# Kernel tuning notes

Measured on AMD Instinct MI355X. Metric: run time of the kernel, lower is better.

## Reference

```python
import jax, jax.numpy as jnp
import numpy as np

B, R, L, K, E, H, V, QV = 256, 6, 10, 49, 300, 512, 2001, 10000


def _lstm_dir(x, Wih, Whh, bih, bhh):
    # x: [N, L, E]; returns final hidden state [N, H] (PyTorch gate order i,f,g,o)
    N = x.shape[0]
    Hd = Whh.shape[1]
    b = bih + bhh

    def step(carry, xt):
        h, c = carry
        gates = xt @ Wih.T + h @ Whh.T + b
        i, f, g, o = jnp.split(gates, 4, axis=-1)
        c = jax.nn.sigmoid(f) * c + jax.nn.sigmoid(i) * jnp.tanh(g)
        h = jax.nn.sigmoid(o) * jnp.tanh(c)
        return (h, c), None

    init = (jnp.zeros((N, Hd), x.dtype), jnp.zeros((N, Hd), x.dtype))
    (h, _), _ = jax.lax.scan(step, init, jnp.swapaxes(x, 0, 1))
    return h


def setup_inputs() -> dict:
    key = jax.random.key(0)
    ks = jax.random.split(key, 40)
    s = 0.02
    d = {}
    d['img'] = jax.random.normal(ks[0], (B * R, K, H), jnp.float32)
    d['role_qs'] = jax.random.randint(ks[1], (B, R, L), 0, QV, jnp.int64)
    d['qword_emb'] = jax.random.normal(ks[2], (QV, E), jnp.float32) * s
    d['lstm_Wih_f'] = jax.random.normal(ks[3], (4 * H, E), jnp.float32) * s
    d['lstm_Whh_f'] = jax.random.normal(ks[4], (4 * H, H), jnp.float32) * s
    d['lstm_bih_f'] = jnp.zeros((4 * H,), jnp.float32)
    d['lstm_bhh_f'] = jnp.zeros((4 * H,), jnp.float32)
    d['lstm_Wih_b'] = jax.random.normal(ks[5], (4 * H, E), jnp.float32) * s
    d['lstm_Whh_b'] = jax.random.normal(ks[6], (4 * H, H), jnp.float32) * s
    d['lstm_bih_b'] = jnp.zeros((4 * H,), jnp.float32)
    d['lstm_bhh_b'] = jnp.zeros((4 * H,), jnp.float32)
    d['proj_W'] = jax.random.normal(ks[7], (H, 2 * H), jnp.float32) * s
    d['proj_b'] = jnp.zeros((H,), jnp.float32)
    d['vatt_vW'] = jax.random.normal(ks[8], (H, H), jnp.float32) * s
    d['vatt_vb'] = jnp.zeros((H,), jnp.float32)
    d['vatt_qW'] = jax.random.normal(ks[9], (H, H), jnp.float32) * s
    d['vatt_qb'] = jnp.zeros((H,), jnp.float32)
    d['vatt_oW'] = jax.random.normal(ks[10], (1, H), jnp.float32) * s
    d['vatt_ob'] = jnp.zeros((1,), jnp.float32)
    d['qnet_W'] = jax.random.normal(ks[11], (H, H), jnp.float32) * s
    d['qnet_b'] = jnp.zeros((H,), jnp.float32)
    d['vnet_W'] = jax.random.normal(ks[12], (H, H), jnp.float32) * s
    d['vnet_b'] = jnp.zeros((H,), jnp.float32)
    d['cls_W1'] = jax.random.normal(ks[13], (2 * H, H), jnp.float32) * s
    d['cls_b1'] = jnp.zeros((2 * H,), jnp.float32)
    d['cls_W2'] = jax.random.normal(ks[14], (V, 2 * H), jnp.float32) * s
    d['cls_b2'] = jnp.zeros((V,), jnp.float32)
    d['g0_W'] = jax.random.normal(ks[15], (H, 2 * H), jnp.float32) * s
    d['g0_b'] = jnp.zeros((H,), jnp.float32)
    d['g1_W'] = jax.random.normal(ks[16], (H, H), jnp.float32) * s
    d['g1_b'] = jnp.zeros((H,), jnp.float32)
    d['g2_W'] = jax.random.normal(ks[17], (H, H), jnp.float32) * s
    d['g2_b'] = jnp.zeros((H,), jnp.float32)
    d['g3_W'] = jax.random.normal(ks[18], (H, H), jnp.float32) * s
    d['g3_b'] = jnp.zeros((H,), jnp.float32)
    d['f0_W'] = jax.random.normal(ks[19], (H, H), jnp.float32) * s
    d['f0_b'] = jnp.zeros((H,), jnp.float32)
    d['f1_W'] = jax.random.normal(ks[20], (H, H), jnp.float32) * s
    d['f1_b'] = jnp.zeros((H,), jnp.float32)
    return d


def _forward(img, qword_emb,
             lstm_Wih_f, lstm_Whh_f, lstm_bih_f, lstm_bhh_f,
             lstm_Wih_b, lstm_Whh_b, lstm_bih_b, lstm_bhh_b,
             proj_W, proj_b, vatt_vW, vatt_vb, vatt_qW, vatt_qb, vatt_oW, vatt_ob,
             qnet_W, qnet_b, vnet_W, vnet_b, cls_W1, cls_b1, cls_W2, cls_b2,
             g0_W, g0_b, g1_W, g1_b, g2_W, g2_b, g3_W, g3_b,
             f0_W, f0_b, f1_W, f1_b, role_qs):
    relu = jax.nn.relu
    bsz, roles = role_qs.shape[0], role_qs.shape[1]
    toks = role_qs.reshape(-1, role_qs.shape[-1])          # [B*R, L]
    w_emb = qword_emb[toks]                                 # [B*R, L, E]
    # bidirectional LSTM final hidden states
    h_f = _lstm_dir(w_emb, lstm_Wih_f, lstm_Whh_f, lstm_bih_f, lstm_bhh_f)
    h_b = _lstm_dir(w_emb[:, ::-1, :], lstm_Wih_b, lstm_Whh_b, lstm_bih_b, lstm_bhh_b)
    q_emb = jnp.concatenate([h_f, h_b], axis=-1) @ proj_W.T + proj_b   # [B*R, H]
    # top-down attention over image regions
    v_proj = relu(img @ vatt_vW.T + vatt_vb)                # [B*R, K, H]
    q_proj = relu(q_emb @ vatt_qW.T + vatt_qb)              # [B*R, H]
    att_logits = (v_proj * q_proj[:, None, :]) @ vatt_oW.T + vatt_ob  # [B*R, K, 1]
    att = jax.nn.softmax(att_logits, axis=1)
    v_emb = jnp.sum(att * img, axis=1)                      # [B*R, H]
    # joint representation + answer classifier
    q_repr = relu(q_emb @ qnet_W.T + qnet_b)
    v_repr = relu(v_emb @ vnet_W.T + vnet_b)
    joint_repr = q_repr * v_repr                            # [B*R, H]
    logits = relu(joint_repr @ cls_W1.T + cls_b1) @ cls_W2.T + cls_b2  # [B*R, V]
    # relation network over pairwise role representations
    jr = joint_repr.reshape(bsz, roles, -1)                 # [B, R, H]
    r1 = jnp.broadcast_to(jr[:, None, :, :], (bsz, roles, roles, jr.shape[-1]))
    r2 = jnp.broadcast_to(jr[:, :, None, :], (bsz, roles, roles, jr.shape[-1]))
    cat = jnp.concatenate([r1, r2], axis=-1).reshape(-1, 2 * jr.shape[-1])  # [B*R*R, 2H]
    g = relu(cat @ g0_W.T + g0_b)
    g = relu(g @ g1_W.T + g1_b)
    g = relu(g @ g2_W.T + g2_b)
    g = relu(g @ g3_W.T + g3_b)
    g = g.reshape(bsz, roles * roles, -1).sum(axis=1)       # [B, H]
    rec = relu(g @ f0_W.T + f0_b) @ f1_W.T + f1_b           # [B, H]
    rec = rec / jnp.sqrt(jnp.sum(rec * rec, axis=1, keepdims=True))  # l2norm
    return logits, rec


def reference(img, role_qs, qword_emb,
              lstm_Wih_f, lstm_Whh_f, lstm_bih_f, lstm_bhh_f,
              lstm_Wih_b, lstm_Whh_b, lstm_bih_b, lstm_bhh_b,
              proj_W, proj_b, vatt_vW, vatt_vb, vatt_qW, vatt_qb, vatt_oW, vatt_ob,
              qnet_W, qnet_b, vnet_W, vnet_b, cls_W1, cls_b1, cls_W2, cls_b2,
              g0_W, g0_b, g1_W, g1_b, g2_W, g2_b, g3_W, g3_b,
              f0_W, f0_b, f1_W, f1_b):
    return _forward(img, qword_emb,
                    lstm_Wih_f, lstm_Whh_f, lstm_bih_f, lstm_bhh_f,
                    lstm_Wih_b, lstm_Whh_b, lstm_bih_b, lstm_bhh_b,
                    proj_W, proj_b, vatt_vW, vatt_vb, vatt_qW, vatt_qb, vatt_oW, vatt_ob,
                    qnet_W, qnet_b, vnet_W, vnet_b, cls_W1, cls_b1, cls_W2, cls_b2,
                    g0_W, g0_b, g1_W, g1_b, g2_W, g2_b, g3_W, g3_b,
                    f0_W, f0_b, f1_W, f1_b, role_qs)
```

## Files before the change

kernel.cpp:

```cpp
#include <hip/hip_runtime.h>
#include <hip/hip_bf16.h>
#include <math.h>

typedef __attribute__((ext_vector_type(8))) short short8;
typedef __attribute__((ext_vector_type(4))) float f32x4;

#define KTILE 32
#define LSTR 40
#define LSTR64 72

__device__ __forceinline__ short8 cvt8(const float* x) {
    short8 r;
#pragma unroll
    for (int i = 0; i < 8; ++i) {
        __hip_bfloat16 b = __float2bfloat16(x[i]);
        r[i] = *reinterpret_cast<const short*>(&b);
    }
    return r;
}
__device__ __forceinline__ float bf2f(short s) {
    unsigned int u = ((unsigned int)(unsigned short)s) << 16;
    return __uint_as_float(u);
}
__device__ __forceinline__ void gload16(const void* g, void* l) {
// ... 50 lines not shown
#pragma unroll
        for (int n = 0; n < 2; ++n) acc[m][n] = (f32x4){0.f, 0.f, 0.f, 0.f};

    short8 aS0, aS1, wS;
    auto loadA = [&](int t) {
        constexpr int AE = (BM == 128) ? 16 : 8;
        const int k0 = t * KTILE + kA;
        if (k0 + AE <= k1) {
            if (abits & 1) {
                const short* p = A1b + (size_t)rgA * lda1 + k0;
                aS0 = *(const short8*)p;
                if constexpr (BM == 128) aS1 = *(const short8*)(p + 8);
            } else {
                const float* p = A1f + (size_t)rgA * lda1 + k0;
                float4 v0 = *(const float4*)p, v1 = *(const float4*)(p + 4);
                float t0[8] = {v0.x, v0.y, v0.z, v0.w, v1.x, v1.y, v1.z, v1.w};
                aS0 = cvt8(t0);
                if constexpr (BM == 128) {
                    float4 v2 = *(const float4*)(p + 8), v3 = *(const float4*)(p + 12);
                    float t1[8] = {v2.x, v2.y, v2.z, v2.w, v3.x, v3.y, v3.z, v3.w};
                    aS1 = cvt8(t1);
                }
            }
        } else if (k0 >= k1 && k0 + AE <= Ktot) {
            const int kk = k0 - k1;
            if (abits & 2) {
                const short* p = A2b + (size_t)rgA * lda2 + kk;
                aS0 = *(const short8*)p;
                if constexpr (BM == 128) aS1 = *(const short8*)(p + 8);
            } else {
                const float* p = A2f + (size_t)rgA * lda2 + kk;
                float4 v0 = *(const float4*)p, v1 = *(const float4*)(p + 4);
                float t0[8] = {v0.x, v0.y, v0.z, v0.w, v1.x, v1.y, v1.z, v1.w};
                aS0 = cvt8(t0);
                if constexpr (BM == 128) {
                    float4 v2 = *(const float4*)(p + 8), v3 = *(const float4*)(p + 12);
                    float t1[8] = {v2.x, v2.y, v2.z, v2.w, v3.x, v3.y, v3.z, v3.w};
                    aS1 = cvt8(t1);
                }
            }
        } else {
            float tmp[(BM == 128) ? 16 : 8];
#pragma unroll
            for (int e = 0; e < ((BM == 128) ? 16 : 8); ++e) {
                const int kg = k0 + e;
                float v = 0.f;
                if (kg < k1) v = (abits & 1) ? bf2f(A1b[(size_t)rgA * lda1 + kg]) : A1f[(size_t)rgA * lda1 + kg];
                else if (kg < Ktot) v = (abits & 2) ? bf2f(A2b[(size_t)rgA * lda2 + (kg - k1)]) : A2f[(size_t)rgA * lda2 + (kg - k1)];
                tmp[e] = v;
            }
            aS0 = cvt8(tmp);
            if constexpr (BM == 128) aS1 = cvt8(tmp + 8);
        }
    };
    auto loadW = [&](int t) {
        const int k0 = t * KTILE + kW;
        if (k0 + 8 <= k1) {
            wS = *(const short8*)&W1[(size_t)ngW * ldw1 + k0];
        } else if (k0 >= k1 && k0 + 8 <= Ktot) {
            wS = *(const short8*)&W2[(size_t)ngW * ldw2 + (k0 - k1)];
        } else {
            short8 w;
#pragma unroll
            for (int e = 0; e < 8; ++e) {
                const int kg = k0 + e;
                w[e] = (kg < k1) ? W1[(size_t)ngW * ldw1 + kg]
                                 : ((kg < Ktot) ? W2[(size_t)ngW * ldw2 + (kg - k1)] : (short)0);
            }
            wS = w;
        }
    };
    auto writeS = [&](int buf) {
        *(short8*)&sA[buf][rowA][kA] = aS0;
        if constexpr (BM == 128) *(short8*)&sA[buf][rowA][kA + 8] = aS1;
        *(short8*)&sB[buf][rowW][kW] = wS;
    };

    loadA(0); loadW(0); writeS(0);
    __syncthreads();
    for (int t = 0; t < nt; ++t) {
        const int cur = t & 1;
        if (t + 1 < nt) { loadA(t + 1); loadW(t + 1); }
        short8 af[MF], bfv[2];
#pragma unroll
        for (int m = 0; m < MF; ++m)
            af[m] = *(const short8*)&sA[cur][wr + (m << 4) + l15][lh << 3];
#pragma unroll
        for (int n = 0; n < 2; ++n)
            bfv[n] = *(const short8*)&sB[cur][wc + (n << 4) + l15][lh << 3];
#pragma unroll
        for (int m = 0; m < MF; ++m)
#pragma unroll
            for (int n = 0; n < 2; ++n)
                acc[m][n] = __builtin_amdgcn_mfma_f32_16x16x32_bf16(af[m], bfv[n], acc[m][n], 0, 0, 0);
        if (t + 1 < nt) writeS(cur ^ 1);
        __syncthreads();
    }

    if (mode == 0) {
#pragma unroll
        for (int m = 0; m < MF; ++m) {
#pragma unroll
            for (int j = 0; j < 4; ++j) {
                const int r = m0 + wr + (m << 4) + (lh << 2) + j;
                if (r >= M) continue;
#pragma unroll
                for (int n = 0; n < 2; ++n) {
                    const int c = n0 + wc + (n << 4) + l15;
                    if (c >= N) continue;
                    float v = acc[m][n][j];
                    if (bias1) v += bias1[c];
                    if (do_relu) v = fmaxf(v, 0.f);
                    if (mulvec) v *= mulvec[c];
                    if (mul) v *= mul[(size_t)r * ldc + c];
                    if (c_bf16) {
                        __hip_bfloat16 b = __float2bfloat16(v);
                        ((short*)C)[(size_t)r * ldc + c] = *(short*)&b;
                    } else {
                        C[(size_t)r * ldc + c] = v;
                    }
                }
            }
        }
    } else {
#pragma unroll
        for (int m = 0; m < MF; ++m) {
#pragma unroll
            for (int j = 0; j < 4; ++j) {
                const int rloc = wr + (m << 4) + (lh << 2) + j;
                const int r = m0 + rloc;
                const size_t sqbase = (size_t)(r / 49) * ldc;
                float s = 0.f;
#pragma unroll
                for (int n = 0; n < 2; ++n) {
                    const int c = n0 + wc + (n << 4) + l15;
                    float v = acc[m][n][j] + bias1[c];
                    v = fmaxf(v, 0.f);
                    s += v * mul[sqbase + c];
                }
                s += __shfl_xor(s, 1, 64);
                s += __shfl_xor(s, 2, 64);
                s += __shfl_xor(s, 4, 64);
                s += __shfl_xor(s, 8, 64);
                if (l15 == 0) sred[rloc][wc >> 5] = s;
            }
        }
        __syncthreads();
        if (tid < BM)
            C[(size_t)(m0 + tid) * 8 + ch8] = sred[tid][0] + sred[tid][1];
    }
}

__global__ __launch_bounds__(256)
void attn_logits3_kernel(const short* __restrict__ imgb, const short* __restrict__ vW,
                         const float* __restrict__ vb, const float* __restrict__ swq,
                         float* __restrict__ partial)
{
    __shared__ short sA[2][128][64];
    __shared__ short sB[2][64][64];
    __shared__ float sred[128][2];
    const int tid = threadIdx.x;
    const int lane = tid & 63, wave = tid >> 6;
    const int xcd = blockIdx.x & 7;
    const int gi = xcd * 588 + (blockIdx.x >> 3);
    const int m0 = (gi >> 3) << 7;
    const int ch8 = gi & 7;
    const int n0 = ch8 << 6;
    const int wr = (wave >> 1) << 6;
    const int wc = (wave & 1) << 5;
    const int l15 = lane & 15, lh = lane >> 4;
    const int lr = lane >> 3;
    const int sc = (lane & 7) ^ lr;

    f32x4 acc[4][2];
#pragma unroll
    for (int m = 0; m < 4; ++m)
#pragma unroll
        for (int n = 0; n < 2; ++n) acc[m][n] = (f32x4){0.f, 0.f, 0.f, 0.f};

    auto stage = [&](int t, int buf) {
        const int kb = t << 6;
#pragma unroll
        for (int j = 0; j < 4; ++j) {
            const int r0 = (wave << 5) + (j << 3);
            const int grow = m0 + r0 + lr;
            gload16(imgb + (size_t)grow * 512 + kb + (sc << 3), &sA[buf][r0][0]);
        }
#pragma unroll
        for (int j = 0; j < 2; ++j) {
            const int r0 = (wave << 4) + (j << 3);
            const int grow = n0 + r0 + lr;
            gload16(vW + (size_t)grow * 512 + kb + (sc << 3), &sB[buf][r0][0]);
        }
    };

    stage(0, 0);
    __syncthreads();
    for (int t = 0; t < 8; ++t) {
        const int cur = t & 1;
        if (t + 1 < 8) stage(t + 1, cur ^ 1);
#pragma unroll
        for (int kk = 0; kk < 2; ++kk) {
            const int rd = (((kk << 2) + lh) ^ (l15 & 7)) << 3;
            short8 af[4], bfv[2];
#pragma unroll
            for (int m = 0; m < 4; ++m)
                af[m] = *(const short8*)&sA[cur][wr + (m << 4) + l15][rd];
#pragma unroll
            for (int n = 0; n < 2; ++n)
                bfv[n] = *(const short8*)&sB[cur][wc + (n << 4) + l15][rd];
#pragma unroll
            for (int m = 0; m < 4; ++m)
#pragma unroll
                for (int n = 0; n < 2; ++n)
                    acc[m][n] = __builtin_amdgcn_mfma_f32_16x16x32_bf16(af[m], bfv[n], acc[m][n], 0, 0, 0);
        }
        __syncthreads();
    }

#pragma unroll
    for (int m = 0; m < 4; ++m) {
#pragma unroll
        for (int j = 0; j < 4; ++j) {
            const int rloc = wr + (m << 4) + (lh << 2) + j;
            const int r = m0 + rloc;
            const size_t sqbase = (size_t)(r / 49) * 512;
            float s = 0.f;
#pragma unroll
            for (int n = 0; n < 2; ++n) {
                const int c = n0 + wc + (n << 4) + l15;
                float v = acc[m][n][j] + vb[c];
                v = fmaxf(v, 0.f);
                s += v * swq[sqbase + c];
            }
            s += __shfl_xor(s, 1, 64);
            s += __shfl_xor(s, 2, 64);
            s += __shfl_xor(s, 4, 64);
            s += __shfl_xor(s, 8, 64);
            if (l15 == 0) sred[rloc][wc >> 5] = s;
        }
    }
    __syncthreads();
    if (tid < 128)
        partial[(size_t)(m0 + tid) * 8 + ch8] = sred[tid][0] + sred[tid][1];
}

__global__ __launch_bounds__(256)
void mfma_gemm64_kernel(const float* __restrict__ A1f, int lda1, int k1,
                        const short* __restrict__ W1, int ldw1,
                        const float* __restrict__ A2f, int lda2, int k2,
                        const short* __restrict__ W2, int ldw2,
                        const float* __restrict__ bias1,
                        const float* __restrict__ mulvec, const float* __restrict__ mul,
                        float* __restrict__ C, int ldc, int M, int N,
                        int do_relu, int abits, int c_bf16)
{
    __shared__ short sA[2][64][LSTR64];
    __shared__ short sB[2][64][LSTR64];
    const int tid = threadIdx.x;
    const int m0 = blockIdx.y << 6, n0 = blockIdx.x << 6;
    const short* A1b = (const short*)A1f;
    const short* A2b = (const short*)A2f;
    const int Ktot = k1 + k2;
    const int nt = (Ktot + 63) >> 6;
    const int lane = tid & 63, wave = tid >> 6;
    const int wr = (wave >> 1) << 5, wc = (wave & 1) << 5;
    const int l15 = lane & 15, lh = lane >> 4;
    const int srow = tid >> 2, skq = (tid & 3) << 4;
    const int rgA = min(m0 + srow, M - 1);
    const int ngW = min(n0 + srow, N - 1);

    f32x4 acc[2][2];
#pragma unroll
    for (int m = 0; m < 2; ++m)
#pragma unroll
        for (int n = 0; n < 2; ++n) acc[m][n] = (f32x4){0.f, 0.f, 0.f, 0.f};

    short8 aS0, aS1, wS0, wS1;
    auto loadA = [&](int t) {
        const int k0 = (t << 6) + skq;
        if (k0 + 16 <= k1) {
            if (abits & 1) {
                const short* p = A1b + (size_t)rgA * lda1 + k0;
                aS0 = *(const short8*)p; aS1 = *(const short8*)(p + 8);
            } else {
                const float* p = A1f + (size_t)rgA * lda1 + k0;
                float4 v0 = *(const float4*)p, v1 = *(const float4*)(p + 4);
                float4 v2 = *(const float4*)(p + 8), v3 = *(const float4*)(p + 12);
                float t0[8] = {v0.x, v0.y, v0.z, v0.w, v1.x, v1.y, v1.z, v1.w};
                float t1[8] = {v2.x, v2.y, v2.z, v2.w, v3.x, v3.y, v3.z, v3.w};
                aS0 = cvt8(t0); aS1 = cvt8(t1);
            }
        } else if (k0 >= k1 && k0 + 16 <= Ktot) {
            const int kk = k0 - k1;
            if (abits & 2) {
                const short* p = A2b + (size_t)rgA * lda2 + kk;
                aS0 = *(const short8*)p; aS1 = *(const short8*)(p + 8);
            } else {
                const float* p = A2f + (size_t)rgA * lda2 + kk;
                float4 v0 = *(const float4*)p, v1 = *(const float4*)(p + 4);
                float4 v2 = *(const float4*)(p + 8), v3 = *(const float4*)(p + 12);
                float t0[8] = {v0.x, v0.y, v0.z, v0.w, v1.x, v1.y, v1.z, v1.w};
                float t1[8] = {v2.x, v2.y, v2.z, v2.w, v3.x, v3.y, v3.z, v3.w};
                aS0 = cvt8(t0); aS1 = cvt8(t1);
            }
        } else {
            float tmp[16];
#pragma unroll
            for (int e = 0; e < 16; ++e) {
                const int kg = k0 + e;
                float v = 0.f;
                if (kg < k1) v = (abits & 1) ? bf2f(A1b[(size_t)rgA * lda1 + kg]) : A1f[(size_t)rgA * lda1 + kg];
                else if (kg < Ktot) v = (abits & 2) ? bf2f(A2b[(size_t)rgA * lda2 + (kg - k1)]) : A2f[(size_t)rgA * lda2 + (kg - k1)];
                tmp[e] = v;
            }
            aS0 = cvt8(tmp); aS1 = cvt8(tmp + 8);
        }
    };
    auto loadW = [&](int t) {
        const int k0 = (t << 6) + skq;
        if (k0 + 16 <= k1) {
            const short* p = W1 + (size_t)ngW * ldw1 + k0;
            wS0 = *(const short8*)p; wS1 = *(const short8*)(p + 8);
        } else if (k0 >= k1 && k0 + 16 <= Ktot) {
            const short* p = W2 + (size_t)ngW * ldw2 + (k0 - k1);
            wS0 = *(const short8*)p; wS1 = *(const short8*)(p + 8);
        } else {
            short8 w0, w1;
#pragma unroll
            for (int e = 0; e < 16; ++e) {
                const int kg = k0 + e;
                short v = (kg < k1) ? W1[(size_t)ngW * ldw1 + kg]
                                    : ((kg < Ktot) ? W2[(size_t)ngW * ldw2 + (kg - k1)] : (short)0);
                if (e < 8) w0[e] = v; else w1[e - 8] = v;
            }
            wS0 = w0; wS1 = w1;
        }
    };
    auto writeS = [&](int buf) {
        *(short8*)&sA[buf][srow][skq] = aS0;
        *(short8*)&sA[buf][srow][skq + 8] = aS1;
        *(short8*)&sB[buf][srow][skq] = wS0;
        *(short8*)&sB[buf][srow][skq + 8] = wS1;
    };

    loadA(0); loadW(0); writeS(0);
    __syncthreads();
    for (int t = 0; t < nt; ++t) {
        const int cur = t & 1;
        if (t + 1 < nt) { loadA(t + 1); loadW(t + 1); }
#pragma unroll
        for (int kk = 0; kk < 2; ++kk) {
            short8 af[2], bfv[2];
#pragma unroll
            for (int m = 0; m < 2; ++m)
                af[m] = *(const short8*)&sA[cur][wr + (m << 4) + l15][(kk << 5) + (lh << 3)];
#pragma unroll
            for (int n = 0; n < 2; ++n)
                bfv[n] = *(const short8*)&sB[cur][wc + (n << 4) + l15][(kk << 5) + (lh << 3)];
#pragma unroll
            for (int m = 0; m < 2; ++m)
#pragma unroll
                for (int n = 0; n < 2; ++n)
                    acc[m][n] = __builtin_amdgcn_mfma_f32_16x16x32_bf16(af[m], bfv[n], acc[m][n], 0, 0, 0);
        }
        if (t + 1 < nt) writeS(cur ^ 1);
        __syncthreads();
    }

#pragma unroll
    for (int m = 0; m < 2; ++m) {
#pragma unroll
        for (int j = 0; j < 4; ++j) {
            const int r = m0 + wr + (m << 4) + (lh << 2) + j;
            if (r >= M) continue;
#pragma unroll
            for (int n = 0; n < 2; ++n) {
                const int c = n0 + wc + (n << 4) + l15;
                if (c >= N) continue;
                float v = acc[m][n][j];
                if (bias1) v += bias1[c];
                if (do_relu) v = fmaxf(v, 0.f);
                if (mulvec) v *= mulvec[c];
                if (mul) v *= mul[(size_t)r * ldc + c];
                if (c_bf16) {
                    __hip_bfloat16 b = __float2bfloat16(v);
                    ((short*)C)[(size_t)r * ldc + c] = *(short*)&b;
                } else {
                    C[(size_t)r * ldc + c] = v;
                }
            }
        }
    }
}

__global__ __launch_bounds__(256)
void wcvt_kernel(const float* __restrict__ proj, const float* __restrict__ qW,
                 const float* __restrict__ vW, const float* __restrict__ qnet,
                 const float* __restrict__ vnet, const float* __restrict__ cls1,
                 const float* __restrict__ cls2, const float* __restrict__ g0,
                 const float* __restrict__ g1, const float* __restrict__ g2,
                 const float* __restrict__ g3, const float* __restrict__ f0,
                 const float* __restrict__ f1, short* __restrict__ dst)
{
    size_t idx = ((size_t)blockIdx.x * 256 + threadIdx.x) * 8;
    if (idx >= 5981184) return;
    const float* s;
    if (idx < 524288) s = proj + idx;
    else if (idx < 786432) s = qW + (idx - 524288);
    else if (idx < 1048576) s = vW + (idx - 786432);
    else if (idx < 1310720) s = qnet + (idx - 1048576);
    else if (idx < 1572864) s = vnet + (idx - 1310720);
    else if (idx < 2097152) s = cls1 + (idx - 1572864);
    else if (idx < 4146176) s = cls2 + (idx - 2097152);
    else if (idx < 4670464) {
        size_t li = idx - 4146176;
        int c = (int)(li >> 9), k = (int)(li & 511);
        s = (c < 512) ? g0 + (size_t)c * 1024 + k
                      : g0 + (size_t)(c - 512) * 1024 + 512 + k;
    }
    else if (idx < 4932608) s = g1 + (idx - 4670464);
    else if (idx < 5194752) s = g2 + (idx - 4932608);
    else if (idx < 5456896) s = g3 + (idx - 5194752);
    else if (idx < 5719040) s = f0 + (idx - 5456896);
    else s = f1 + (idx - 5719040);
    float4 a = *(const float4*)s, b = *(const float4*)(s + 4);
    float t[8] = {a.x, a.y, a.z, a.w, b.x, b.y, b.z, b.w};
    *(short8*)(dst + idx) = cvt8(t);
}

__global__ __launch_bounds__(256)
void lstm_reorder_kernel(const float* __restrict__ Wih, const float* __restrict__ Whh,
                         const float* __restrict__ bih, const float* __restrict__ bhh,
                         short* __restrict__ Wbf, float* __restrict__ bias_perm)
{
    int id = blockIdx.x * 256 + threadIdx.x;
    int c = id >> 9, k = id & 511;
    int src = (c & 3) * 512 + (c >> 2);
    {
        __hip_bfloat16 b = __float2bfloat16(Whh[(size_t)src * 512 + k]);
        Wbf[(size_t)c * 832 + k] = *(short*)&b;
    }
    if (k < 300) {
        __hip_bfloat16 b = __float2bfloat16(Wih[(size_t)src * 300 + k]);
        Wbf[(size_t)c * 832 + 512 + k] = *(short*)&b;
    } else if (k < 320) {
        Wbf[(size_t)c * 832 + 512 + k] = 0;
    }
    if (k == 0) bias_perm[c] = bih[src] + bhh[src];
}

__global__ __launch_bounds__(256)
void embcvt_kernel(const float* __restrict__ qword, short* __restrict__ embp)
{
    int id = blockIdx.x * 256 + threadIdx.x;
    if (id >= 3200000) return;
    int r = id / 320, c = id % 320;
    float v = (c < 300) ? qword[(size_t)r * 300 + c] : 0.f;
    __hip_bfloat16 b = __float2bfloat16(v);
    embp[id] = *(short*)&b;
}

__global__ __launch_bounds__(256)
void lstm_step6_kernel(const short* __restrict__ hF_in, const short* __restrict__ hB_in,
                       const short* __restrict__ WbfF, const short* __restrict__ WbfB,
                       const float* __restrict__ biasF, const float* __restrict__ biasB,
                       const short* __restrict__ embp, const int* __restrict__ toks,
                       int tF, int tB, int first,
                       short* __restrict__ hF_out, short* __restrict__ hB_out,
                       float* __restrict__ cF, float* __restrict__ cB)
{
    __shared__ short sA[2][64][64];
    __shared__ short sB[2][64][64];
    const int dir = blockIdx.z;
    const short* h_in = dir ? hB_in : hF_in;
    const short* Wbf  = dir ? WbfB : WbfF;
    const float* bias_perm = dir ? biasB : biasF;
    short* h_out  = dir ? hB_out : hF_out;
    float* cstate = dir ? cB : cF;
    const int tt = dir ? tB : tF;

    const int tid = threadIdx.x;
    const int m0 = blockIdx.y << 6;
    const int n0 = blockIdx.x << 6;
    const int lane = tid & 63, wave = tid >> 6;
    const int wr = (wave >> 1) << 5, wc = (wave & 1) << 5;
    const int l15 = lane & 15, lh = lane >> 4;
    const int lr = lane >> 3;
    const int sc = (lane & 7) ^ lr;

    f32x4 acc[2][2];
#pragma unroll
    for (int m = 0; m < 2; ++m)
#pragma unroll
        for (int n = 0; n < 2; ++n) acc[m][n] = (f32x4){0.f, 0.f, 0.f, 0.f};

    auto stage = [&](int t, int buf) {
#pragma unroll
        for (int j = 0; j < 2; ++j) {
            const int r0 = (wave << 4) + (j << 3);
            const int grow = m0 + r0 + lr;
            const short* g;
            if (t < 8) {
                g = h_in + (size_t)grow * 512 + (t << 6) + (sc << 3);
            } else {
                const int ar = toks[grow * 10 + tt];
                g = embp + (size_t)ar * 320 + ((t - 8) << 6) + (sc << 3);
            }
            gload16(g, &sA[buf][r0][0]);
        }
#pragma unroll
        for (int j = 0; j < 2; ++j) {
            const int r0 = (wave << 4) + (j << 3);
            const int grow = n0 + r0 + lr;
            gload16(Wbf + (size_t)grow * 832 + (t << 6) + (sc << 3), &sB[buf][r0][0]);
        }
    };

    stage(0, 0);
    __syncthreads();
    for (int t = 0; t < 13; ++t) {
        const int cur = t & 1;
        if (t + 1 < 13) stage(t + 1, cur ^ 1);
#pragma unroll
        for (int kk = 0; kk < 2; ++kk) {
            const int rd = (((kk << 2) + lh) ^ (l15 & 7)) << 3;
            short8 af[2], bfv[2];
#pragma unroll
            for (int m = 0; m < 2; ++m)
                af[m] = *(const short8*)&sA[cur][wr + (m << 4) + l15][rd];
#pragma unroll
            for (int n = 0; n < 2; ++n)
                bfv[n] = *(const short8*)&sB[cur][wc + (n << 4) + l15][rd];
#pragma unroll
            for (int m = 0; m < 2; ++m)
#pragma unroll
                for (int n = 0; n < 2; ++n)
                    acc[m][n] = __builtin_amdgcn_mfma_f32_16x16x32_bf16(af[m], bfv[n], acc[m][n], 0, 0, 0);
        }
        __syncthreads();
    }

#pragma unroll
    for (int n = 0; n < 2; ++n) {
        const int ccol = n0 + wc + (n << 4) + l15;
        const float bb = bias_perm[ccol];
        const int u = ccol >> 2;
#pragma unroll
        for (int m = 0; m < 2; ++m) {
#pragma unroll
            for (int j = 0; j < 4; ++j) {
                const int r = m0 + wr + (m << 4) + (lh << 2) + j;
                float v = acc[m][n][j] + bb;
                const int base = lane & ~3;
                float gi = __shfl(v, base, 64);
                float gf = __shfl(v, base | 1, 64);
                float gg = __shfl(v, base | 2, 64);
                float go = __shfl(v, base | 3, 64);
                if ((lane & 3) == 0) {
                    float si = 1.f / (1.f + expf(-gi));
                    float sf = 1.f / (1.f + expf(-gf));
                    float so = 1.f / (1.f + expf(-go));
                    size_t idx = ((size_t)r << 9) + u;
                    float cold = first ? 0.f : cstate[idx];
                    float cv = sf * cold + si * tanhf(gg);
                    cstate[idx] = cv;
                    float hv = so * tanhf(cv);
                    __hip_bfloat16 b = __float2bfloat16(hv);
                    h_out[idx] = *(short*)&b;
                }
            }
        }
    }
}

__global__ __launch_bounds__(256)
void lstm_step4_kernel(const short* __restrict__ hF_in, const short* __restrict__ hB_in,
                       const short* __restrict__ WbfF, const short* __restrict__ WbfB,
                       const float* __restrict__ biasF, const float* __restrict__ biasB,
                       const float* __restrict__ emb, const int* __restrict__ toks,
                       int tF, int tB, int first,
                       short* __restrict__ hF_out, short* __restrict__ hB_out,
                       float* __restrict__ cF, float* __restrict__ cB)
{
    __shared__ short sA[2][64][LSTR64];
    __shared__ short sB[2][64][LSTR64];
    const int dir = blockIdx.z;
    const short* h_in = dir ? hB_in : hF_in;
    const short* Wbf  = dir ? WbfB : WbfF;
    const float* bias_perm = dir ? biasB : biasF;
    short* h_out  = dir ? hB_out : hF_out;
    float* cstate = dir ? cB : cF;
    const int tt = dir ? tB : tF;

    const int tid = threadIdx.x;
    const int m0 = blockIdx.y << 6;
    const int n0 = blockIdx.x << 6;
    const int lane = tid & 63, wave = tid >> 6;
    const int wr = (wave >> 1) << 5, wc = (wave & 1) << 5;
    const int l15 = lane & 15, lh = lane >> 4;
    const int srow = tid >> 2, skq = (tid & 3) << 4;
    const int rgA = m0 + srow;
    const int ngW = n0 + srow;
    const int nt = 13;
    const int arow = toks[rgA * 10 + tt];

    f32x4 acc[2][2];
#pragma unroll
    for (int m = 0; m < 2; ++m)
#pragma unroll
        for (int n = 0; n < 2; ++n) acc[m][n] = (f32x4){0.f, 0.f, 0.f, 0.f};

    short8 aS0, aS1, wS0, wS1;
    auto loadA = [&](int t) {
        const int k0 = (t << 6) + skq;
        if (k0 + 16 <= 512) {
            if (first) { short8 z = {0,0,0,0,0,0,0,0}; aS0 = z; aS1 = z; }
            else {
                const short* p = h_in + (size_t)rgA * 512 + k0;
                aS0 = *(const short8*)p; aS1 = *(const short8*)(p + 8);
            }
        } else if (k0 >= 512 && k0 + 16 <= 812) {
            const float* p = emb + (size_t)arow * 300 + (k0 - 512);
            float4 v0 = *(const float4*)p, v1 = *(const float4*)(p + 4);
            float4 v2 = *(const float4*)(p + 8), v3 = *(const float4*)(p + 12);
            float t0[8] = {v0.x, v0.y, v0.z, v0.w, v1.x, v1.y, v1.z, v1.w};
            float t1[8] = {v2.x, v2.y, v2.z, v2.w, v3.x, v3.y, v3.z, v3.w};
            aS0 = cvt8(t0); aS1 = cvt8(t1);
        } else {
            float tmp[16];
#pragma unroll
            for (int e = 0; e < 16; ++e) {
                const int kg = k0 + e;
                float v = 0.f;
                if (kg < 512) v = first ? 0.f : bf2f(h_in[(size_t)rgA * 512 + kg]);
                else if (kg < 812) v = emb[(size_t)arow * 300 + (kg - 512)];
                tmp[e] = v;
            }
            aS0 = cvt8(tmp); aS1 = cvt8(tmp + 8);
        }
    };
    auto loadW = [&](int t) {
        const short* p = Wbf + (size_t)ngW * 832 + (t << 6) + skq;
        wS0 = *(const short8*)p; wS1 = *(const short8*)(p + 8);
    };
    auto writeS = [&](int buf) {
        *(short8*)&sA[buf][srow][skq] = aS0;
        *(short8*)&sA[buf][srow][skq + 8] = aS1;
        *(short8*)&sB[buf][srow][skq] = wS0;
        *(short8*)&sB[buf][srow][skq + 8] = wS1;
    };

    loadA(0); loadW(0); writeS(0);
    __syncthreads();
    for (int t = 0; t < nt; ++t) {
        const int cur = t & 1;
        if (t + 1 < nt) { loadA(t + 1); loadW(t + 1); }
#pragma unroll
        for (int kk = 0; kk < 2; ++kk) {
            short8 af[2], bfv[2];
#pragma unroll
            for (int m = 0; m < 2; ++m)
                af[m] = *(const short8*)&sA[cur][wr + (m << 4) + l15][(kk << 5) + (lh << 3)];
#pragma unroll
            for (int n = 0; n < 2; ++n)
                bfv[n] = *(const short8*)&sB[cur][wc + (n << 4) + l15][(kk << 5) + (lh << 3)];
#pragma unroll
            for (int m = 0; m < 2; ++m)
// ... 90 lines not shown
    }
    ((float2*)(v_emb + (size_t)n * 512))[tid] = s2;
}

__global__ __launch_bounds__(256)
void g0build_kernel(const float* __restrict__ PQ, const float* __restrict__ b0,
                    short* __restrict__ g0)
{
    int id = blockIdx.x * 256 + threadIdx.x;
    int cc = id & 511;
    int r = id >> 9;
    int j = r % 6;
    int t = r / 6;
    int i = t % 6;
    int b = t / 6;
    float v = PQ[(size_t)(b * 6 + j) * 1024 + cc] + PQ[(size_t)(b * 6 + i) * 1024 + 512 + cc] + b0[cc];
    v = fmaxf(v, 0.f);
    __hip_bfloat16 h = __float2bfloat16(v);
    g0[id] = *(short*)&h;
}

__global__ __launch_bounds__(256)
void gsum_kernel(const short* __restrict__ g, float* __restrict__ out)
{
    int id = blockIdx.x * 256 + threadIdx.x;
    int b = id >> 9, hh = id & 511;
    const short* p = g + (size_t)b * 36 * 512 + hh;
    float s = 0.f;
#pragma unroll
    for (int i = 0; i < 36; ++i) s += bf2f(p[i * 512]);
    out[id] = s;
}

__global__ __launch_bounds__(256)
void l2norm_kernel(const float* __restrict__ in, float* __restrict__ out)
{
    int b = blockIdx.x;
    int tid = threadIdx.x;
    float v0 = in[(size_t)b * 512 + tid];
    float v1 = in[(size_t)b * 512 + 256 + tid];
    float s = v0 * v0 + v1 * v1;
#pragma unroll
    for (int off = 32; off; off >>= 1) s += __shfl_down(s, off, 64);
    __shared__ float ps[4];
    if ((tid & 63) == 0) ps[tid >> 6] = s;
    __syncthreads();
    float tot = ps[0] + ps[1] + ps[2] + ps[3];
    float inv = 1.f / sqrtf(tot);
    out[(size_t)b * 512 + tid] = v0 * inv;
    out[(size_t)b * 512 + 256 + tid] = v1 * inv;
}

extern "C" void kernel_launch(void* const* d_in, const int* in_sizes, int n_in,
                              void* d_out, int out_size, void* d_ws, size_t ws_size,
                              hipStream_t stream)
{
    (void)in_sizes; (void)n_in; (void)out_size;
    const float* img    = (const float*)d_in[0];
    const int*   toks   = (const int*)d_in[1];
    const float* qword  = (const float*)d_in[2];
    const float* Wih_f  = (const float*)d_in[3];
    const float* Whh_f  = (const float*)d_in[4];
    const float* bih_f  = (const float*)d_in[5];
    const float* bhh_f  = (const float*)d_in[6];
    const float* Wih_b  = (const float*)d_in[7];
    const float* Whh_b  = (const float*)d_in[8];
    const float* bih_b  = (const float*)d_in[9];
    const float* bhh_b  = (const float*)d_in[10];
    const float* proj_W = (const float*)d_in[11];
    const float* proj_b = (const float*)d_in[12];
    const float* vatt_vW = (const float*)d_in[13];
    const float* vatt_vb = (const float*)d_in[14];
    const float* vatt_qW = (const float*)d_in[15];
    const float* vatt_qb = (const float*)d_in[16];
    const float* vatt_oW = (const float*)d_in[17];
    const float* qnet_W = (const float*)d_in[19];
    const float* qnet_b = (const float*)d_in[20];
    const float* vnet_W = (const float*)d_in[21];
    const float* vnet_b = (const float*)d_in[22];
    const float* cls_W1 = (const float*)d_in[23];
    const float* cls_b1 = (const float*)d_in[24];
    const float* cls_W2 = (const float*)d_in[25];
    const float* cls_b2 = (const float*)d_in[26];
    const float* g0_W   = (const float*)d_in[27];
    const float* g0_b   = (const float*)d_in[28];
    const float* g1_W   = (const float*)d_in[29];
    const float* g1_b   = (const float*)d_in[30];
    const float* g2_W   = (const float*)d_in[31];
    const float* g2_b   = (const float*)d_in[32];
    const float* g3_W   = (const float*)d_in[33];
    const float* g3_b   = (const float*)d_in[34];
    const float* f0_W   = (const float*)d_in[35];
    const float* f0_b   = (const float*)d_in[36];
    const float* f1_W   = (const float*)d_in[37];
    const float* f1_b   = (const float*)d_in[38];

    float* out_logits = (float*)d_out;
    float* out_rec    = (float*)d_out + 1536 * 2001;

    const size_t FB = 786432;
    float* zone = (float*)d_ws;
    float* gA    = zone;
    float* gB    = zone + 4718592;
    float* hid1  = zone + 9437184;
    float* PQb   = zone + 11010048;
    float* gsumb = zone + 12582912;
    float* f0o   = zone + 12713984;
    float* rectb = zone + 12845056;
    float* p = zone + 12976128;
    auto alloc = [&](size_t nf) { float* q = p; p += nf; return q; };
    float* hP0   = alloc(FB);
    float* hP2   = alloc(FB);
    float* joint = alloc(FB);
    float* partial = alloc(602112);
    short* WbfF  = (short*)alloc(851968);
    short* WbfB  = (short*)alloc(851968);
    float* biasF = alloc(2048);
    float* biasB = alloc(2048);
    const size_t TOPF = 17645568;
    short* wb = (short*)(zone + TOPF);
    short* projbf = wb;
    short* qWbf   = wb + 524288;
    short* vWbf   = wb + 786432;
    short* qnetbf = wb + 1048576;
    short* vnetbf = wb + 1310720;
    short* cls1bf = wb + 1572864;
    short* cls2bf = wb + 2097152;
    short* wpqbf  = wb + 4146176;
    short* g1bf   = wb + 4670464;
    short* g2bf   = wb + 4932608;
    short* g3bf   = wb + 5194752;
    short* f0bf   = wb + 5456896;
    short* f1bf   = wb + 5719040;
    const size_t WEND = TOPF + 2990592;
    const size_t IMGBF = 19267584;
    const size_t EMBPF = 1600000;
    const bool useimgbf = ws_size >= (WEND + IMGBF) * sizeof(float);
    const bool useglds  = ws_size >= (WEND + IMGBF + EMBPF) * sizeof(float);
    short* imgbf = (short*)(zone + WEND);
    short* embp  = (short*)(zone + WEND + IMGBF);
    short* hP1 = (short*)gA;
    short* hP3 = (short*)(gA + FB);
    float* cF  = gA + 2 * FB;
    float* cB  = gA + 3 * FB;
    float* q_emb  = PQb;
    float* swq    = hid1;
    float* q_repr = gA;
    float* v_emb  = gA + FB;

    auto gemm = [&](const float* A1, int lda1, int k1, const short* W1, int ldw1,
                    const float* A2, int lda2, int k2, const short* W2, int ldw2,
                    const float* b1, const float* mv, const float* mulp,
                    float* Cp, int ldc, int M, int N, int relu, int abits, int cbf) {
        if (M >= 4096) {
            dim3 g((N + 63) / 64, (M + 127) / 128);
            hipLaunchKernelGGL(HIP_KERNEL_NAME(mfma_gemm_t<128>), g, dim3(256), 0, stream,
                               A1, lda1, k1, W1, ldw1, A2, lda2, k2, W2, ldw2,
                               b1, mv, mulp, Cp, ldc, M, N, relu, 0, abits, cbf);
        } else {
            dim3 g((N + 63) / 64, (M + 63) / 64);
            hipLaunchKernelGGL(mfma_gemm64_kernel, g, dim3(256), 0, stream,
                               A1, lda1, k1, W1, ldw1, A2, lda2, k2, W2, ldw2,
                               b1, mv, mulp, Cp, ldc, M, N, relu, abits, cbf);
        }
    };

    const int NR = 1536;
    hipLaunchKernelGGL(lstm_reorder_kernel, dim3(4096), dim3(256), 0, stream,
                       Wih_f, Whh_f, bih_f, bhh_f, WbfF, biasF);
    hipLaunchKernelGGL(lstm_reorder_kernel, dim3(4096), dim3(256), 0, stream,
                       Wih_b, Whh_b, bih_b, bhh_b, WbfB, biasB);
    hipLaunchKernelGGL(wcvt_kernel, dim3(2921), dim3(256), 0, stream,
                       proj_W, vatt_qW, vatt_vW, qnet_W, vnet_W, cls_W1, cls_W2,
                       g0_W, g1_W, g2_W, g3_W, f0_W, f1_W, wb);
    if (useimgbf)
        hipLaunchKernelGGL(imgcvt_kernel, dim3(18816), dim3(256), 0, stream, img, imgbf);

    if (useglds) {
        hipLaunchKernelGGL(embcvt_kernel, dim3(12500), dim3(256), 0, stream, qword, embp);
        hipMemsetAsync(hP0, 0, FB * sizeof(short), stream);
        hipMemsetAsync(hP2, 0, FB * sizeof(short), stream);
        short *fi = (short*)hP0, *fo = hP1, *bi = (short*)hP2, *bo = hP3;
        for (int t = 0; t < 10; ++t) {
            hipLaunchKernelGGL(lstm_step6_kernel, dim3(32, 24, 2), dim3(256), 0, stream,
                               fi, bi, WbfF, WbfB, biasF, biasB, embp, toks, t, 9 - t,
                               (t == 0) ? 1 : 0, fo, bo, cF, cB);
            short* tmp = fi; fi = fo; fo = tmp;
            tmp = bi; bi = bo; bo = tmp;
        }
    } else {
        short *fi = (short*)hP0, *fo = hP1, *bi = (short*)hP2, *bo = hP3;
        for (int t = 0; t < 10; ++t) {
            hipLaunchKernelGGL(lstm_step4_kernel, dim3(32, 24, 2), dim3(256), 0, stream,
                               fi, bi, WbfF, WbfB, biasF, biasB, qword, toks, t, 9 - t,
                               (t == 0) ? 1 : 0, fo, bo, cF, cB);
            short* tmp = fi; fi = fo; fo = tmp;
            tmp = bi; bi = bo; bo = tmp;
        }
    }

    gemm(hP0, 512, 512, projbf, 1024, hP2, 512, 512, projbf + 512, 1024,
         proj_b, nullptr, nullptr, q_emb, 512, NR, 512, 0, 3, 1);
    gemm(q_emb, 512, 512, qWbf, 512, nullptr, 0, 0, nullptr, 0,
         vatt_qb, vatt_oW, nullptr, swq, 512, NR, 512, 1, 1, 0);
    if (useimgbf) {
        hipLaunchKernelGGL(attn_logits3_kernel, dim3(4704), dim3(256), 0, stream,
                           imgbf, vWbf, vatt_vb, swq, partial);
    } else {
        hipLaunchKernelGGL(HIP_KERNEL_NAME(mfma_gemm_t<128>), dim3(4704), dim3(256), 0, stream,
                           img, 512, 512, vWbf, 512,
                           (const float*)nullptr, 0, 0, (const short*)nullptr, 0,
                           vatt_vb, (const float*)nullptr, swq,
                           partial, 512, 75264, 512, 0, 1, 0, 0);
    }
    hipLaunchKernelGGL(attn_vemb_kernel, dim3(1536), dim3(256), 0, stream,
                       partial, img, useimgbf ? imgbf : (const short*)nullptr, v_emb);
    gemm(q_emb, 512, 512, qnetbf, 512, nullptr, 0, 0, nullptr, 0,
         qnet_b, nullptr, nullptr, q_repr, 512, NR, 512, 1, 1, 0);
    gemm(v_emb, 512, 512, vnetbf, 512, nullptr, 0, 0, nullptr, 0,
         vnet_b, nullptr, q_repr, joint, 512, NR, 512, 1, 0, 1);
    gemm(joint, 512, 512, cls1bf, 512, nullptr, 0, 0, nullptr, 0,
         cls_b1, nullptr, nullptr, hid1, 1024, NR, 1024, 1, 1, 1);
    gemm(hid1, 1024, 1024, cls2bf, 1024, nullptr, 0, 0, nullptr, 0,
         cls_b2, nullptr, nullptr, out_logits, 2001, NR, 2001, 0, 1, 0);
    gemm(joint, 512, 512, wpqbf, 512, nullptr, 0, 0, nullptr, 0,
         nullptr, nullptr, nullptr, PQb, 1024, NR, 1024, 0, 1, 0);
    hipLaunchKernelGGL(g0build_kernel, dim3(18432), dim3(256), 0, stream,
                       PQb, g0_b, (short*)gA);
    gemm(gA, 512, 512, g1bf, 512, nullptr, 0, 0, nullptr, 0,
         g1_b, nullptr, nullptr, gB, 512, 9216, 512, 1, 1, 1);
    gemm(gB, 512, 512, g2bf, 512, nullptr, 0, 0, nullptr, 0,
         g2_b, nullptr, nullptr, gA, 512, 9216, 512, 1, 1, 1);
    gemm(gA, 512, 512, g3bf, 512, nullptr, 0, 0, nullptr, 0,
         g3_b, nullptr, nullptr, gB, 512, 9216, 512, 1, 1, 1);
    hipLaunchKernelGGL(gsum_kernel, dim3(512), dim3(256), 0, stream, (const short*)gB, gsumb);
    gemm(gsumb, 512, 512, f0bf, 512, nullptr, 0, 0, nullptr, 0,
         f0_b, nullptr, nullptr, f0o, 512, 256, 512, 1, 0, 0);
    gemm(f0o, 512, 512, f1bf, 512, nullptr, 0, 0, nullptr, 0,
         f1_b, nullptr, nullptr, rectb, 512, 256, 512, 0, 0, 0);
    hipLaunchKernelGGL(l2norm_kernel, dim3(256), dim3(256), 0, stream, rectb, out_rec);
}
```

Before: 787.5 us.

## Route bf16-input GEMMs through direct global-to-LDS kernels and shrink attention tiles

Adds two GEMM kernels that take bf16 operands and stage tiles with direct global-to-LDS 16-byte loads and XOR swizzling, in 64x64 and 128x64 variants. Most mid-size linear layers (proj, qatt, qnet, cls1, PQ) and the three 9216-row relation MLP layers now use them instead of the generic float/bf16 GEMM path. The attention-logit kernel switches from 128-row to 64-row tiles, doubling the grid to improve occupancy and load balance. The generic gemm lambda now always uses the 64-tile kernel. This relies on the producers already writing bf16 and on M and N being multiples of the tile sizes.

```diff
diff --git a/kernel.cpp b/kernel.cpp
--- a/kernel.cpp
+++ b/kernel.cpp
@@ -226,45 +226,211 @@
 }
 
 __global__ __launch_bounds__(256)
-void attn_logits3_kernel(const short* __restrict__ imgb, const short* __restrict__ vW,
+void mfma_glds64_kernel(const short* __restrict__ A1, const short* __restrict__ A2,
+                        int lda, int k1, const short* __restrict__ W, int ldw,
+                        const float* __restrict__ bias, const float* __restrict__ mulvec,
+                        float* __restrict__ C, int ldc, int Ktot, int do_relu, int c_bf16)
+{
+    __shared__ short sA[2][64][64];
+    __shared__ short sB[2][64][64];
+    const int tid = threadIdx.x;
+    const int m0 = blockIdx.y << 6, n0 = blockIdx.x << 6;
+    const int lane = tid & 63, wave = tid >> 6;
+    const int wr = (wave >> 1) << 5, wc = (wave & 1) << 5;
+    const int l15 = lane & 15, lh = lane >> 4;
+    const int lr = lane >> 3;
+    const int sc = (lane & 7) ^ lr;
+    const int nt = Ktot >> 6;
+    const int t1 = k1 >> 6;
+
+    f32x4 acc[2][2];
+#pragma unroll
+    for (int m = 0; m < 2; ++m)
+#pragma unroll
+        for (int n = 0; n < 2; ++n) acc[m][n] = (f32x4){0.f, 0.f, 0.f, 0.f};
+
+    auto stage = [&](int t, int buf) {
+        const short* Ab = (t < t1) ? A1 : A2;
+        const int kb = ((t < t1) ? t : (t - t1)) << 6;
+#pragma unroll
+        for (int j = 0; j < 2; ++j) {
+            const int r0 = (wave << 4) + (j << 3);
+            gload16(Ab + (size_t)(m0 + r0 + lr) * lda + kb + (sc << 3), &sA[buf][r0][0]);
+        }
+#pragma unroll
+        for (int j = 0; j < 2; ++j) {
+            const int r0 = (wave << 4) + (j << 3);
+            gload16(W + (size_t)(n0 + r0 + lr) * ldw + (t << 6) + (sc << 3), &sB[buf][r0][0]);
+        }
+    };
+
+    stage(0, 0);
+    __syncthreads();
+    for (int t = 0; t < nt; ++t) {
+        const int cur = t & 1;
+        if (t + 1 < nt) stage(t + 1, cur ^ 1);
+#pragma unroll
+        for (int kk = 0; kk < 2; ++kk) {
+            const int rd = (((kk << 2) + lh) ^ (l15 & 7)) << 3;
+            short8 af[2], bfv[2];
+#pragma unroll
+            for (int m = 0; m < 2; ++m)
+                af[m] = *(const short8*)&sA[cur][wr + (m << 4) + l15][rd];
+#pragma unroll
+            for (int n = 0; n < 2; ++n)
+                bfv[n] = *(const short8*)&sB[cur][wc + (n << 4) + l15][rd];
+#pragma unroll
+            for (int m = 0; m < 2; ++m)
+#pragma unroll
+                for (int n = 0; n < 2; ++n)
+                    acc[m][n] = __builtin_amdgcn_mfma_f32_16x16x32_bf16(af[m], bfv[n], acc[m][n], 0, 0, 0);
+        }
+        __syncthreads();
+    }
+
+#pragma unroll
+    for (int m = 0; m < 2; ++m) {
+#pragma unroll
+        for (int j = 0; j < 4; ++j) {
+            const int r = m0 + wr + (m << 4) + (lh << 2) + j;
+#pragma unroll
+            for (int n = 0; n < 2; ++n) {
+                const int c = n0 + wc + (n << 4) + l15;
+                float v = acc[m][n][j];
+                if (bias) v += bias[c];
+                if (do_relu) v = fmaxf(v, 0.f);
+                if (mulvec) v *= mulvec[c];
+                if (c_bf16) {
+                    __hip_bfloat16 b = __float2bfloat16(v);
+                    ((short*)C)[(size_t)r * ldc + c] = *(short*)&b;
+                } else {
+                    C[(size_t)r * ldc + c] = v;
+                }
+            }
+        }
+    }
+}
+
+__global__ __launch_bounds__(256)
+void mfma_glds128_kernel(const short* __restrict__ A, int lda,
+                         const short* __restrict__ W, int ldw,
+                         const float* __restrict__ bias,
+                         float* __restrict__ C, int ldc, int Ktot, int do_relu, int c_bf16)
+{
+    __shared__ short sA[2][128][64];
+    __shared__ short sB[2][64][64];
+    const int tid = threadIdx.x;
+    const int m0 = blockIdx.y << 7, n0 = blockIdx.x << 6;
+    const int lane = tid & 63, wave = tid >> 6;
+    const int wr = (wave >> 1) << 6, wc = (wave & 1) << 5;
+    const int l15 = lane & 15, lh = lane >> 4;
+    const int lr = lane >> 3;
+    const int sc = (lane & 7) ^ lr;
+    const int nt = Ktot >> 6;
+
+    f32x4 acc[4][2];
+#pragma unroll
+    for (int m = 0; m < 4; ++m)
+#pragma unroll
+        for (int n = 0; n < 2; ++n) acc[m][n] = (f32x4){0.f, 0.f, 0.f, 0.f};
+
+    auto stage = [&](int t, int buf) {
+        const int kb = t << 6;
+#pragma unroll
+        for (int j = 0; j < 4; ++j) {
+            const int r0 = (wave << 5) + (j << 3);
+            gload16(A + (size_t)(m0 + r0 + lr) * lda + kb + (sc << 3), &sA[buf][r0][0]);
+        }
+#pragma unroll
+        for (int j = 0; j < 2; ++j) {
+            const int r0 = (wave << 4) + (j << 3);
+            gload16(W + (size_t)(n0 + r0 + lr) * ldw + kb + (sc << 3), &sB[buf][r0][0]);
+        }
+    };
+
+    stage(0, 0);
+    __syncthreads();
+    for (int t = 0; t < nt; ++t) {
+        const int cur = t & 1;
+        if (t + 1 < nt) stage(t + 1, cur ^ 1);
+#pragma unroll
+        for (int kk = 0; kk < 2; ++kk) {
+            const int rd = (((kk << 2) + lh) ^ (l15 & 7)) << 3;
+            short8 af[4], bfv[2];
+#pragma unroll
+            for (int m = 0; m < 4; ++m)
+                af[m] = *(const short8*)&sA[cur][wr + (m << 4) + l15][rd];
+#pragma unroll
+            for (int n = 0; n < 2; ++n)
+                bfv[n] = *(const short8*)&sB[cur][wc + (n << 4) + l15][rd];
+#pragma unroll
+            for (int m = 0; m < 4; ++m)
+#pragma unroll
+                for (int n = 0; n < 2; ++n)
+                    acc[m][n] = __builtin_amdgcn_mfma_f32_16x16x32_bf16(af[m], bfv[n], acc[m][n], 0, 0, 0);
+        }
+        __syncthreads();
+    }
+
+#pragma unroll
+    for (int m = 0; m < 4; ++m) {
+#pragma unroll
+        for (int j = 0; j < 4; ++j) {
+            const int r = m0 + wr + (m << 4) + (lh << 2) + j;
+#pragma unroll
+            for (int n = 0; n < 2; ++n) {
+                const int c = n0 + wc + (n << 4) + l15;
+                float v = acc[m][n][j];
+                if (bias) v += bias[c];
+                if (do_relu) v = fmaxf(v, 0.f);
+                if (c_bf16) {
+                    __hip_bfloat16 b = __float2bfloat16(v);
+                    ((short*)C)[(size_t)r * ldc + c] = *(short*)&b;
+                } else {
+                    C[(size_t)r * ldc + c] = v;
+                }
+            }
+        }
+    }
+}
+
+__global__ __launch_bounds__(256)
+void attn_logits4_kernel(const short* __restrict__ imgb, const short* __restrict__ vW,
                          const float* __restrict__ vb, const float* __restrict__ swq,
                          float* __restrict__ partial)
 {
-    __shared__ short sA[2][128][64];
+    __shared__ short sA[2][64][64];
     __shared__ short sB[2][64][64];
-    __shared__ float sred[128][2];
+    __shared__ float sred[64][2];
     const int tid = threadIdx.x;
     const int lane = tid & 63, wave = tid >> 6;
     const int xcd = blockIdx.x & 7;
-    const int gi = xcd * 588 + (blockIdx.x >> 3);
-    const int m0 = (gi >> 3) << 7;
+    const int gi = xcd * 1176 + (blockIdx.x >> 3);
+    const int m0 = (gi >> 3) << 6;
     const int ch8 = gi & 7;
     const int n0 = ch8 << 6;
-    const int wr = (wave >> 1) << 6;
-    const int wc = (wave & 1) << 5;
+    const int wr = (wave >> 1) << 5, wc = (wave & 1) << 5;
     const int l15 = lane & 15, lh = lane >> 4;
     const int lr = lane >> 3;
     const int sc = (lane & 7) ^ lr;
 
-    f32x4 acc[4][2];
-#pragma unroll
-    for (int m = 0; m < 4; ++m)
+    f32x4 acc[2][2];
+#pragma unroll
+    for (int m = 0; m < 2; ++m)
 #pragma unroll
         for (int n = 0; n < 2; ++n) acc[m][n] = (f32x4){0.f, 0.f, 0.f, 0.f};
 
     auto stage = [&](int t, int buf) {
         const int kb = t << 6;
 #pragma unroll
-        for (int j = 0; j < 4; ++j) {
-            const int r0 = (wave << 5) + (j << 3);
-            const int grow = m0 + r0 + lr;
-            gload16(imgb + (size_t)grow * 512 + kb + (sc << 3), &sA[buf][r0][0]);
-        }
-#pragma unroll
         for (int j = 0; j < 2; ++j) {
             const int r0 = (wave << 4) + (j << 3);
-            const int grow = n0 + r0 + lr;
-            gload16(vW + (size_t)grow * 512 + kb + (sc << 3), &sB[buf][r0][0]);
+            gload16(imgb + (size_t)(m0 + r0 + lr) * 512 + kb + (sc << 3), &sA[buf][r0][0]);
+        }
+#pragma unroll
+        for (int j = 0; j < 2; ++j) {
+            const int r0 = (wave << 4) + (j << 3);
+            gload16(vW + (size_t)(n0 + r0 + lr) * 512 + kb + (sc << 3), &sB[buf][r0][0]);
         }
     };
 
@@ -276,15 +442,15 @@
 #pragma unroll
         for (int kk = 0; kk < 2; ++kk) {
             const int rd = (((kk << 2) + lh) ^ (l15 & 7)) << 3;
-            short8 af[4], bfv[2];
-#pragma unroll
-            for (int m = 0; m < 4; ++m)
+            short8 af[2], bfv[2];
+#pragma unroll
+            for (int m = 0; m < 2; ++m)
                 af[m] = *(const short8*)&sA[cur][wr + (m << 4) + l15][rd];
 #pragma unroll
             for (int n = 0; n < 2; ++n)
                 bfv[n] = *(const short8*)&sB[cur][wc + (n << 4) + l15][rd];
 #pragma unroll
-            for (int m = 0; m < 4; ++m)
+            for (int m = 0; m < 2; ++m)
 #pragma unroll
                 for (int n = 0; n < 2; ++n)
                     acc[m][n] = __builtin_amdgcn_mfma_f32_16x16x32_bf16(af[m], bfv[n], acc[m][n], 0, 0, 0);
@@ -293,7 +459,7 @@
     }
 
 #pragma unroll
-    for (int m = 0; m < 4; ++m) {
+    for (int m = 0; m < 2; ++m) {
 #pragma unroll
         for (int j = 0; j < 4; ++j) {
             const int rloc = wr + (m << 4) + (lh << 2) + j;
@@ -315,7 +481,7 @@
         }
     }
     __syncthreads();
-    if (tid < 128)
+    if (tid < 64)
         partial[(size_t)(m0 + tid) * 8 + ch8] = sred[tid][0] + sred[tid][1];
 }
 
@@ -586,8 +752,7 @@
 #pragma unroll
         for (int j = 0; j < 2; ++j) {
             const int r0 = (wave << 4) + (j << 3);
-            const int grow = n0 + r0 + lr;
-            gload16(Wbf + (size_t)grow * 832 + (t << 6) + (sc << 3), &sB[buf][r0][0]);
+            gload16(Wbf + (size_t)(n0 + r0 + lr) * 832 + (t << 6) + (sc << 3), &sB[buf][r0][0]);
         }
     };
 
@@ -984,17 +1149,17 @@
                     const float* A2, int lda2, int k2, const short* W2, int ldw2,
                     const float* b1, const float* mv, const float* mulp,
                     float* Cp, int ldc, int M, int N, int relu, int abits, int cbf) {
-        if (M >= 4096) {
-            dim3 g((N + 63) / 64, (M + 127) / 128);
-            hipLaunchKernelGGL(HIP_KERNEL_NAME(mfma_gemm_t<128>), g, dim3(256), 0, stream,
-                               A1, lda1, k1, W1, ldw1, A2, lda2, k2, W2, ldw2,
-                               b1, mv, mulp, Cp, ldc, M, N, relu, 0, abits, cbf);
-        } else {
-            dim3 g((N + 63) / 64, (M + 63) / 64);
-            hipLaunchKernelGGL(mfma_gemm64_kernel, g, dim3(256), 0, stream,
-                               A1, lda1, k1, W1, ldw1, A2, lda2, k2, W2, ldw2,
-                               b1, mv, mulp, Cp, ldc, M, N, relu, abits, cbf);
-        }
+        dim3 g((N + 63) / 64, (M + 63) / 64);
+        hipLaunchKernelGGL(mfma_gemm64_kernel, g, dim3(256), 0, stream,
+                           A1, lda1, k1, W1, ldw1, A2, lda2, k2, W2, ldw2,
+                           b1, mv, mulp, Cp, ldc, M, N, relu, abits, cbf);
+    };
+    auto gemmg = [&](const short* A1, const short* A2, int lda, int k1,
+                     const short* W, int ldw, const float* b1, const float* mv,
+                     float* Cp, int ldc, int M, int N, int Ktot, int relu, int cbf) {
+        dim3 g(N >> 6, M >> 6);
+        hipLaunchKernelGGL(mfma_glds64_kernel, g, dim3(256), 0, stream,
+                           A1, A2, lda, k1, W, ldw, b1, mv, Cp, ldc, Ktot, relu, cbf);
     };
 
     const int NR = 1536;
@@ -1031,12 +1196,12 @@
         }
     }
 
-    gemm(hP0, 512, 512, projbf, 1024, hP2, 512, 512, projbf + 512, 1024,
-         proj_b, nullptr, nullptr, q_emb, 512, NR, 512, 0, 3, 1);
-    gemm(q_emb, 512, 512, qWbf, 512, nullptr, 0, 0, nullptr, 0,
-         vatt_qb, vatt_oW, nullptr, swq, 512, NR, 512, 1, 1, 0);
+    gemmg((const short*)hP0, (const short*)hP2, 512, 512, projbf, 1024,
+          proj_b, nullptr, q_emb, 512, NR, 512, 1024, 0, 1);
+    gemmg((const short*)q_emb, nullptr, 512, 512, qWbf, 512,
+          vatt_qb, vatt_oW, swq, 512, NR, 512, 512, 1, 0);
     if (useimgbf) {
-        hipLaunchKernelGGL(attn_logits3_kernel, dim3(4704), dim3(256), 0, stream,
+        hipLaunchKernelGGL(attn_logits4_kernel, dim3(9408), dim3(256), 0, stream,
                            imgbf, vWbf, vatt_vb, swq, partial);
     } else {
         hipLaunchKernelGGL(HIP_KERNEL_NAME(mfma_gemm_t<128>), dim3(4704), dim3(256), 0, stream,
@@ -1047,24 +1212,24 @@
     }
     hipLaunchKernelGGL(attn_vemb_kernel, dim3(1536), dim3(256), 0, stream,
                        partial, img, useimgbf ? imgbf : (const short*)nullptr, v_emb);
-    gemm(q_emb, 512, 512, qnetbf, 512, nullptr, 0, 0, nullptr, 0,
-         qnet_b, nullptr, nullptr, q_repr, 512, NR, 512, 1, 1, 0);
+    gemmg((const short*)q_emb, nullptr, 512, 512, qnetbf, 512,
+          qnet_b, nullptr, q_repr, 512, NR, 512, 512, 1, 0);
     gemm(v_emb, 512, 512, vnetbf, 512, nullptr, 0, 0, nullptr, 0,
          vnet_b, nullptr, q_repr, joint, 512, NR, 512, 1, 0, 1);
-    gemm(joint, 512, 512, cls1bf, 512, nullptr, 0, 0, nullptr, 0,
-         cls_b1, nullptr, nullptr, hid1, 1024, NR, 1024, 1, 1, 1);
+    gemmg((const short*)joint, nullptr, 512, 512, cls1bf, 512,
+          cls_b1, nullptr, hid1, 1024, NR, 1024, 512, 1, 1);
     gemm(hid1, 1024, 1024, cls2bf, 1024, nullptr, 0, 0, nullptr, 0,
          cls_b2, nullptr, nullptr, out_logits, 2001, NR, 2001, 0, 1, 0);
-    gemm(joint, 512, 512, wpqbf, 512, nullptr, 0, 0, nullptr, 0,
-         nullptr, nullptr, nullptr, PQb, 1024, NR, 1024, 0, 1, 0);
+    gemmg((const short*)joint, nullptr, 512, 512, wpqbf, 512,
+          nullptr, nullptr, PQb, 1024, NR, 1024, 512, 0, 0);
     hipLaunchKernelGGL(g0build_kernel, dim3(18432), dim3(256), 0, stream,
                        PQb, g0_b, (short*)gA);
-    gemm(gA, 512, 512, g1bf, 512, nullptr, 0, 0, nullptr, 0,
-         g1_b, nullptr, nullptr, gB, 512, 9216, 512, 1, 1, 1);
-    gemm(gB, 512, 512, g2bf, 512, nullptr, 0, 0, nullptr, 0,
-         g2_b, nullptr, nullptr, gA, 512, 9216, 512, 1, 1, 1);
-    gemm(gA, 512, 512, g3bf, 512, nullptr, 0, 0, nullptr, 0,
-         g3_b, nullptr, nullptr, gB, 512, 9216, 512, 1, 1, 1);
+    hipLaunchKernelGGL(mfma_glds128_kernel, dim3(8, 72), dim3(256), 0, stream,
+                       (const short*)gA, 512, g1bf, 512, g1_b, gB, 512, 512, 1, 1);
+    hipLaunchKernelGGL(mfma_glds128_kernel, dim3(8, 72), dim3(256), 0, stream,
+                       (const short*)gB, 512, g2bf, 512, g2_b, gA, 512, 512, 1, 1);
+    hipLaunchKernelGGL(mfma_glds128_kernel, dim3(8, 72), dim3(256), 0, stream,
+                       (const short*)gA, 512, g3bf, 512, g3_b, gB, 512, 512, 1, 1);
     hipLaunchKernelGGL(gsum_kernel, dim3(512), dim3(256), 0, stream, (const short*)gB, gsumb);
     gemm(gsumb, 512, 512, f0bf, 512, nullptr, 0, 0, nullptr, 0,
          f0_b, nullptr, nullptr, f0o, 512, 256, 512, 1, 0, 0);
```

New measurement: 777.2 us. Within noise of the previous version (-1.3%).
